# Kernel tuning notes

Measured on AMD Instinct MI355X. Metric: run time of the kernel, lower is better.

## Reference

```python
import jax, jax.numpy as jnp
import numpy as np

TAU = 1.5      # lif_tau
V_TH = 1.0     # spikingjelly default v_threshold
EPS = 1e-5     # BatchNorm eps
ALPHA = 4.0    # spikingjelly default sigmoid surrogate alpha

@jax.custom_vjp
def spike_fn(x):
    return (x >= 0.0).astype(x.dtype)

def _spike_fwd(x):
    return spike_fn(x), x

def _spike_bwd(x, g):
    s = jax.nn.sigmoid(ALPHA * x)
    return (g * ALPHA * s * (1.0 - s),)

spike_fn.defvjp(_spike_fwd, _spike_bwd)

def lif(x):
    # x: [T, B, C, N]; hard reset to 0, decay_input=True, detach_reset=True
    def step(v, xt):
        v = v + (xt - v) / TAU
        s = spike_fn(v - V_TH)
        sd = jax.lax.stop_gradient(s)
        v = (1.0 - sd) * v
        return v, s
    _, spikes = jax.lax.scan(step, jnp.zeros_like(x[0]), x)
    return spikes

def bn(x, gamma, beta, mean, var):
    # eval-mode BatchNorm1d over channel dim of [B, C, L]
    inv = gamma * jax.lax.rsqrt(var + EPS)
    return x * inv[None, :, None] + (beta - mean * inv)[None, :, None]

def setup_inputs() -> dict:
    key = jax.random.key(0)
    ks = jax.random.split(key, 13)
    B, C, T, N, H = 8, 256, 4, 4096, 1024
    return {
        "x": jax.random.normal(ks[0], (B, C, T, N), jnp.float32),
        "fc1_w": jax.random.normal(ks[1], (H, C), jnp.float32) * 0.05,
        "fc1_b": jax.random.normal(ks[2], (H,), jnp.float32) * 0.05,
        "fc2_w": jax.random.normal(ks[3], (C, H), jnp.float32) * 0.05,
        "fc2_b": jax.random.normal(ks[4], (C,), jnp.float32) * 0.05,
        "bn1_gamma": jax.random.uniform(ks[5], (H,), jnp.float32, 0.5, 1.5),
        "bn1_beta": jax.random.normal(ks[6], (H,), jnp.float32) * 0.1,
        "bn1_mean": jax.random.normal(ks[7], (H,), jnp.float32) * 0.1,
        "bn1_var": jax.random.uniform(ks[8], (H,), jnp.float32, 0.5, 1.5),
        "bn2_gamma": jax.random.uniform(ks[9], (C,), jnp.float32, 0.5, 1.5),
        "bn2_beta": jax.random.normal(ks[10], (C,), jnp.float32) * 0.1,
        "bn2_mean": jax.random.normal(ks[11], (C,), jnp.float32) * 0.1,
        "bn2_var": jax.random.uniform(ks[12], (C,), jnp.float32, 0.5, 1.5),
    }

def reference(x, fc1_w, fc1_b, fc2_w, fc2_b,
              bn1_gamma, bn1_beta, bn1_mean, bn1_var,
              bn2_gamma, bn2_beta, bn2_mean, bn2_var):
    B, C, T, N = x.shape
    H = fc1_w.shape[0]
    # fc2_bn on raw input, then LIF over T
    h = bn(x.reshape(B, C, T * N), bn2_gamma, bn2_beta, bn2_mean, bn2_var)
    h = h.reshape(B, C, T, N).transpose(2, 0, 1, 3)          # [T,B,C,N]
    h = lif(h).transpose(1, 2, 0, 3).reshape(B, C, T * N)    # [B,C,TN]
    # fc1: 1x1 conv == GEMM over channels
    h = jnp.einsum('hc,bcl->bhl', fc1_w, h) + fc1_b[None, :, None]
    h = bn(h, bn1_gamma, bn1_beta, bn1_mean, bn1_var)
    h = h.reshape(B, H, T, N).transpose(2, 0, 1, 3)          # [T,B,H,N]
    h = lif(h).transpose(1, 2, 0, 3).reshape(B, H, T * N)    # [B,H,TN]
    # fc2
    h = jnp.einsum('ch,bhl->bcl', fc2_w, h) + fc2_b[None, :, None]
    return h.reshape(B, C, T, N)
```

## Files before the change

kernel.cpp:

```cpp
#include <hip/hip_runtime.h>

#define BB 8
#define CC 256
#define TT 4
#define NNv 4096
#define HH 1024
#define LLv (TT*NNv)

typedef short bf16x8 __attribute__((ext_vector_type(8)));
typedef float f32x4 __attribute__((ext_vector_type(4)));

static __device__ __forceinline__ float bfbits2f(unsigned short h) {
    return __uint_as_float(((unsigned int)h) << 16);
}
static __device__ __forceinline__ unsigned short f2bf(float f) {
    unsigned int u = __float_as_uint(f);
    return (unsigned short)((u + 0x7FFFu + ((u >> 16) & 1u)) >> 16);
}
static __device__ __forceinline__ int permpos(int j) { return (j >> 1) + ((j & 1) << 2); }

static __device__ __forceinline__ uint4 spikes8_to_bf16(unsigned long long d) {
    unsigned int lo = (unsigned int)d, hi = (unsigned int)(d >> 32);
    uint4 o;
    o.x = (lo & 0x10001u) * 0x3F80u;
    o.y = (hi & 0x10001u) * 0x3F80u;
    o.z = ((lo >> 8) & 0x10001u) * 0x3F80u;
    o.w = ((hi >> 8) & 0x10001u) * 0x3F80u;
    return o;
}

__global__ __launch_bounds__(256) void k_prep1(const float* __restrict__ w,
                                               unsigned short* __restrict__ wf)
{
    int i = blockIdx.x * 256 + threadIdx.x;
    int h = i >> 8, c = i & 255;
    int ht = h >> 6, hr = h & 63, g = hr >> 4, ln = hr & 15;
    int ko = c >> 6, cr = c & 63, kb = cr >> 5, q = (cr >> 3) & 3, j = c & 7;
    size_t base = (((((size_t)ht * 4 + ko) * 2 + kb) * 4 + g) * 64 + q * 16 + ln) * 8 + permpos(j);
    const size_t WS = 262144;
    float x = w[i];
    unsigned short hi = f2bf(x); float r  = __fsub_rn(x, bfbits2f(hi));
    unsigned short md = f2bf(r); float r2 = __fsub_rn(r, bfbits2f(md));
    unsigned short lo = f2bf(r2);
    wf[base] = hi; wf[WS + base] = md; wf[2 * WS + base] = lo;
}

__global__ __launch_bounds__(256) void k_prep2(const float* __restrict__ w,
                                               unsigned short* __restrict__ wf)
{
    int i = blockIdx.x * 256 + threadIdx.x;
    int c = i >> 10, h = i & 1023;
    int ct = c >> 6, cr = c & 63, g = cr >> 4, ln = cr & 15;
    int ko = h >> 7, hr = h & 127, kb = hr >> 5, q = (hr >> 3) & 3, j = h & 7;
    size_t base = (((((size_t)ct * 8 + ko) * 4 + kb) * 4 + g) * 64 + q * 16 + ln) * 8 + permpos(j);
    const size_t WS = 262144;
    float x = w[i];
    unsigned short hi = f2bf(x); float r = __fsub_rn(x, bfbits2f(hi));
    unsigned short lo = f2bf(r);
    wf[base] = hi; wf[WS + base] = lo;
}

__global__ __launch_bounds__(256) void k_bn2_lif_t(
    const float* __restrict__ x,
    const float* __restrict__ g, const float* __restrict__ be,
    const float* __restrict__ mu, const float* __restrict__ va,
    unsigned char* __restrict__ s1T, int b0)
{
    __shared__ unsigned char ts[TT][64][80];
    int tx = threadIdx.x;
    int n0 = blockIdx.x * 64;
    int c0 = blockIdx.y * 64;
    int bl = blockIdx.z;
    int b  = b0 + bl;
    int cl = tx >> 2, np = tx & 3;
    int c = c0 + cl;
    float rsq = __fdiv_rn(1.0f, __fsqrt_rn(__fadd_rn(va[c], 1e-5f)));
    float inv = __fmul_rn(g[c], rsq);
    float add = __fsub_rn(be[c], __fmul_rn(mu[c], inv));
    size_t xb = ((size_t)(b * CC + c) * TT) * NNv + n0 + np * 16;
    float v[16];
    #pragma unroll
    for (int i = 0; i < 16; i++) v[i] = 0.0f;
    #pragma unroll
    for (int t = 0; t < TT; t++) {
        float4 p[4];
        #pragma unroll
        for (int k = 0; k < 4; k++) p[k] = *(const float4*)(x + xb + (size_t)t * NNv + 4 * k);
        const float* xp = (const float*)p;
        unsigned int ob[4] = {0, 0, 0, 0};
        #pragma unroll
        for (int i = 0; i < 16; i++) {
            float y = __fadd_rn(__fmul_rn(xp[i], inv), add);
            float vv = __fadd_rn(v[i], __fdiv_rn(__fsub_rn(y, v[i]), 1.5f));
            bool sp = vv >= 1.0f;
            v[i] = sp ? 0.0f : vv;
            if (sp) ob[i >> 2] |= 1u << (8 * (i & 3));
        }
        uint4 pk; pk.x = ob[0]; pk.y = ob[1]; pk.z = ob[2]; pk.w = ob[3];
        *(uint4*)&ts[t][cl][np * 16] = pk;
    }
    __syncthreads();
    int nl = tx >> 2, cp = tx & 3;
    #pragma unroll
    for (int t = 0; t < TT; t++) {
        unsigned int u[4];
        #pragma unroll
        for (int kk = 0; kk < 4; kk++) {
            u[kk] = (unsigned int)ts[t][cp * 16 + kk * 4 + 0][nl]
                  | ((unsigned int)ts[t][cp * 16 + kk * 4 + 1][nl] << 8)
                  | ((unsigned int)ts[t][cp * 16 + kk * 4 + 2][nl] << 16)
                  | ((unsigned int)ts[t][cp * 16 + kk * 4 + 3][nl] << 24);
        }
        uint4 pk; pk.x = u[0]; pk.y = u[1]; pk.z = u[2]; pk.w = u[3];
        *(uint4*)(s1T + ((size_t)(bl * TT + t) * NNv + n0 + nl) * CC + c0 + cp * 16) = pk;
    }
}

__global__ __launch_bounds__(256) void k_gemm1_lif(
    const unsigned short* __restrict__ w1f,
    const float* __restrict__ b1,
    const float* __restrict__ g1, const float* __restrict__ be1,
    const float* __restrict__ mu1, const float* __restrict__ va1,
    const unsigned char* __restrict__ s1T, unsigned char* __restrict__ s2T)
{
    __shared__ unsigned short Ss[TT][64][72];
    const int tx = threadIdx.x;
    const int n0 = blockIdx.x * 64;
    const int ht = blockIdx.y;
    const int bl = blockIdx.z;
    const int lane = tx & 63, w = tx >> 6;
    const int q = lane >> 4, ln = lane & 15;
    const int mh = (w & 1) * 32, wn = (w >> 1) * 32;
    const int h0 = ht * 64;
    const size_t WS = 262144;

    f32x4 acc[TT][2][2];
    #pragma unroll
    for (int t = 0; t < TT; t++)
    #pragma unroll
    for (int mi = 0; mi < 2; mi++)
    #pragma unroll
    for (int ni = 0; ni < 2; ni++)
        acc[t][mi][ni] = (f32x4){0.f, 0.f, 0.f, 0.f};

    for (int ko = 0; ko < 4; ko++) {
        __syncthreads();
        #pragma unroll
        for (int i = 0; i < 8; i++) {
            int task = i * 256 + tx;
            int cb = task & 7, nr = (task >> 3) & 63, t = task >> 9;
            unsigned long long d = *(const unsigned long long*)(
                s1T + ((size_t)(bl * TT + t) * NNv + n0 + nr) * CC + ko * 64 + cb * 8);
            *(uint4*)&Ss[t][nr][cb * 8] = spikes8_to_bf16(d);
        }
        __syncthreads();
        #pragma unroll
        for (int kb = 0; kb < 2; kb++) {
            bf16x8 wf[2][3];
            #pragma unroll
            for (int mi = 0; mi < 2; mi++) {
                int gg = (mh >> 4) + mi;
                size_t fbase = (((((size_t)ht * 4 + ko) * 2 + kb) * 4 + gg) * 64 + lane) * 8;
                #pragma unroll
                for (int s = 0; s < 3; s++)
                    wf[mi][s] = *(const bf16x8*)(w1f + s * WS + fbase);
            }
            #pragma unroll
            for (int t = 0; t < TT; t++) {
                bf16x8 sf0 = *(const bf16x8*)&Ss[t][wn + ln][kb * 32 + q * 8];
                bf16x8 sf1 = *(const bf16x8*)&Ss[t][wn + 16 + ln][kb * 32 + q * 8];
                #pragma unroll
                for (int s = 0; s < 3; s++) {
                    acc[t][0][0] = __builtin_amdgcn_mfma_f32_16x16x32_bf16(wf[0][s], sf0, acc[t][0][0], 0, 0, 0);
                    acc[t][0][1] = __builtin_amdgcn_mfma_f32_16x16x32_bf16(wf[0][s], sf1, acc[t][0][1], 0, 0, 0);
                    acc[t][1][0] = __builtin_amdgcn_mfma_f32_16x16x32_bf16(wf[1][s], sf0, acc[t][1][0], 0, 0, 0);
                    acc[t][1][1] = __builtin_amdgcn_mfma_f32_16x16x32_bf16(wf[1][s], sf1, acc[t][1][1], 0, 0, 0);
                }
            }
        }
    }

    #pragma unroll
    for (int mi = 0; mi < 2; mi++) {
        float invr[4], addr_[4], biasr[4];
        #pragma unroll
        for (int r = 0; r < 4; r++) {
            int h = h0 + mh + mi * 16 + q * 4 + r;
            float rsq = __fdiv_rn(1.0f, __fsqrt_rn(__fadd_rn(va1[h], 1e-5f)));
            invr[r] = __fmul_rn(g1[h], rsq);
            addr_[r] = __fsub_rn(be1[h], __fmul_rn(mu1[h], invr[r]));
            biasr[r] = b1[h];
        }
        #pragma unroll
        for (int ni = 0; ni < 2; ni++) {
            int l_n = n0 + wn + ni * 16 + ln;
            float v4[4] = {0.f, 0.f, 0.f, 0.f};
            #pragma unroll
            for (int t = 0; t < TT; t++) {
                unsigned int pk = 0;
                #pragma unroll
                for (int r = 0; r < 4; r++) {
                    float h1 = __fadd_rn(acc[t][mi][ni][r], biasr[r]);
                    float y  = __fadd_rn(__fmul_rn(h1, invr[r]), addr_[r]);
                    float vv = __fadd_rn(v4[r], __fdiv_rn(__fsub_rn(y, v4[r]), 1.5f));
                    bool sp = vv >= 1.0f;
                    v4[r] = sp ? 0.0f : vv;
                    if (sp) pk |= (1u << (8 * r));
                }
                *(unsigned int*)(s2T + ((size_t)bl * LLv + t * NNv + l_n) * HH
                                 + h0 + mh + mi * 16 + q * 4) = pk;
            }
        }
    }
}

__global__ __launch_bounds__(256) void k_gemm2(
    const unsigned short* __restrict__ w2f,
    const float* __restrict__ b2c,
    const unsigned char* __restrict__ s2T, float* __restrict__ outp, int b0)
{
    __shared__ unsigned short Ss[128][136];
    const int tx = threadIdx.x;
    const int l0 = blockIdx.x * 128;
    const int ct = blockIdx.y;
    const int bl = blockIdx.z;
    const int b  = b0 + bl;
    const int lane = tx & 63, w = tx >> 6;
    const int q = lane >> 4, ln = lane & 15;
    const int mc = (w & 1) * 32, wl = (w >> 1) * 64;
    const size_t WS = 262144;

    f32x4 acc[2][4];
    #pragma unroll
    for (int mi = 0; mi < 2; mi++)
    #pragma unroll
    for (int ni = 0; ni < 4; ni++)
        acc[mi][ni] = (f32x4){0.f, 0.f, 0.f, 0.f};

    for (int ko = 0; ko < 8; ko++) {
        __syncthreads();
        #pragma unroll
        for (int i = 0; i < 8; i++) {
            int task = i * 256 + tx;
            int hb = task & 15, lr = task >> 4;
            unsigned long long d = *(const unsigned long long*)(
                s2T + ((size_t)bl * LLv + l0 + lr) * HH + ko * 128 + hb * 8);
            *(uint4*)&Ss[lr][hb * 8] = spikes8_to_bf16(d);
        }
        __syncthreads();
        #pragma unroll
        for (int kb = 0; kb < 4; kb++) {
            bf16x8 wf[2][2];
            #pragma unroll
            for (int mi = 0; mi < 2; mi++) {
                int gg = (mc >> 4) + mi;
                size_t fbase = (((((size_t)ct * 8 + ko) * 4 + kb) * 4 + gg) * 64 + lane) * 8;
                #pragma unroll
                for (int s = 0; s < 2; s++)
                    wf[mi][s] = *(const bf16x8*)(w2f + s * WS + fbase);
            }
            bf16x8 sf[4];
            #pragma unroll
            for (int ni = 0; ni < 4; ni++)
                sf[ni] = *(const bf16x8*)&Ss[wl + ni * 16 + ln][kb * 32 + q * 8];
            #pragma unroll
            for (int s = 0; s < 2; s++)
            #pragma unroll
            for (int mi = 0; mi < 2; mi++)
            #pragma unroll
            for (int ni = 0; ni < 4; ni++)
                acc[mi][ni] = __builtin_amdgcn_mfma_f32_16x16x32_bf16(wf[mi][s], sf[ni], acc[mi][ni], 0, 0, 0);
        }
    }
    #pragma unroll
    for (int mi = 0; mi < 2; mi++)
    #pragma unroll
    for (int r = 0; r < 4; r++) {
        int c = ct * 64 + mc + mi * 16 + q * 4 + r;
        float bias = b2c[c];
        #pragma unroll
        for (int ni = 0; ni < 4; ni++) {
            int l = l0 + wl + ni * 16 + ln;
            outp[((size_t)b * CC + c) * LLv + l] = __fadd_rn(acc[mi][ni][r], bias);
        }
    }
}

extern "C" void kernel_launch(void* const* d_in, const int* in_sizes, int n_in,
                              void* d_out, int out_size, void* d_ws, size_t ws_size,
                              hipStream_t stream) {
    const float* x    = (const float*)d_in[0];
    const float* fc1w = (const float*)d_in[1];
    const float* fc1b = (const float*)d_in[2];
    const float* fc2w = (const float*)d_in[3];
    const float* fc2b = (const float*)d_in[4];
    const float* g1   = (const float*)d_in[5];
    const float* be1  = (const float*)d_in[6];
    const float* mu1  = (const float*)d_in[7];
    const float* va1  = (const float*)d_in[8];
    const float* g2   = (const float*)d_in[9];
    const float* be2  = (const float*)d_in[10];
    const float* mu2  = (const float*)d_in[11];
    const float* va2  = (const float*)d_in[12];

    const size_t WB  = (size_t)(3 + 2) * 262144 * sizeof(unsigned short);
    const size_t S1B = (size_t)TT * NNv * CC;
    const size_t S2B = (size_t)LLv * HH;

    int nbc;
    bool full_s1;
    if      (ws_size >= WB + 8 * S1B + 8 * S2B) { nbc = 8; full_s1 = true;  }
    else if (ws_size >= WB + 8 * S1B + 4 * S2B) { nbc = 4; full_s1 = true;  }
    else if (ws_size >= WB + 8 * S1B + 2 * S2B) { nbc = 2; full_s1 = true;  }
    else if (ws_size >= WB + 8 * S1B + 1 * S2B) { nbc = 1; full_s1 = true;  }
    else                                        { nbc = 1; full_s1 = false; }

    unsigned short* w1f = (unsigned short*)d_ws;
    unsigned short* w2f = w1f + (size_t)3 * 262144;
    unsigned char*  s1T = (unsigned char*)(w2f + (size_t)2 * 262144);
    unsigned char*  s2T = s1T + (full_s1 ? (size_t)8 * S1B : S1B);
    float* outp = (float*)d_out;

    hipLaunchKernelGGL(k_prep1, dim3(1024), dim3(256), 0, stream, fc1w, w1f);
    hipLaunchKernelGGL(k_prep2, dim3(1024), dim3(256), 0, stream, fc2w, w2f);

    if (full_s1) {
        hipLaunchKernelGGL(k_bn2_lif_t, dim3(NNv / 64, CC / 64, BB), dim3(256), 0, stream,
                           x, g2, be2, mu2, va2, s1T, 0);
        for (int b0 = 0; b0 < BB; b0 += nbc) {
            hipLaunchKernelGGL(k_gemm1_lif, dim3(NNv / 64, HH / 64, nbc), dim3(256), 0, stream,
                               w1f, fc1b, g1, be1, mu1, va1, s1T + (size_t)b0 * S1B, s2T);
            hipLaunchKernelGGL(k_gemm2, dim3(LLv / 128, CC / 64, nbc), dim3(256), 0, stream,
                               w2f, fc2b, s2T, outp, b0);
        }
    } else {
        for (int b0 = 0; b0 < BB; ++b0) {
            hipLaunchKernelGGL(k_bn2_lif_t, dim3(NNv / 64, CC / 64, 1), dim3(256), 0, stream,
                               x, g2, be2, mu2, va2, s1T, b0);
            hipLaunchKernelGGL(k_gemm1_lif, dim3(NNv / 64, HH / 64, 1), dim3(256), 0, stream,
                               w1f, fc1b, g1, be1, mu1, va1, s1T, s2T);
            hipLaunchKernelGGL(k_gemm2, dim3(LLv / 128, CC / 64, 1), dim3(256), 0, stream,
                               w2f, fc2b, s2T, outp, b0);
        }
    }
}
```

Measured before the change: 623.7 us.

## Double-buffer spike tiles and prefetch next K slice in both GEMMs

Both GEMM kernels now keep two LDS buffers for the spike tile and load the next K-slice from global memory into registers while the current slice is computed. Each iteration has one barrier instead of two. A custom barrier waits only on LDS counters, so the outstanding global loads stay in flight across it. The cost is doubled LDS use (lower occupancy for the gemm2 tile of about 68KB) and extra registers for the prefetched data.

```diff
diff --git a/kernel.cpp b/kernel.cpp
--- a/kernel.cpp
+++ b/kernel.cpp
@@ -27,6 +27,12 @@
     o.z = ((lo >> 8) & 0x10001u) * 0x3F80u;
     o.w = ((hi >> 8) & 0x10001u) * 0x3F80u;
     return o;
+}
+
+static __device__ __forceinline__ void barrier_keep_vmem() {
+    asm volatile("s_waitcnt lgkmcnt(0)" ::: "memory");
+    __builtin_amdgcn_s_barrier();
+    __builtin_amdgcn_sched_barrier(0);
 }
 
 __global__ __launch_bounds__(256) void k_prep1(const float* __restrict__ w,
@@ -123,7 +129,7 @@
     const float* __restrict__ mu1, const float* __restrict__ va1,
     const unsigned char* __restrict__ s1T, unsigned char* __restrict__ s2T)
 {
-    __shared__ unsigned short Ss[TT][64][72];
+    __shared__ unsigned short Ss[2][TT][64][72];
     const int tx = threadIdx.x;
     const int n0 = blockIdx.x * 64;
     const int ht = blockIdx.y;
@@ -143,17 +149,34 @@
     for (int ni = 0; ni < 2; ni++)
         acc[t][mi][ni] = (f32x4){0.f, 0.f, 0.f, 0.f};
 
+    unsigned long long d[8];
+    #pragma unroll
+    for (int i = 0; i < 8; i++) {
+        int task = i * 256 + tx;
+        int cb = task & 7, nr = (task >> 3) & 63, t = task >> 9;
+        d[i] = *(const unsigned long long*)(
+            s1T + ((size_t)(bl * TT + t) * NNv + n0 + nr) * CC + 0 * 64 + cb * 8);
+    }
+
     for (int ko = 0; ko < 4; ko++) {
-        __syncthreads();
+        const int cur = ko & 1;
         #pragma unroll
         for (int i = 0; i < 8; i++) {
             int task = i * 256 + tx;
             int cb = task & 7, nr = (task >> 3) & 63, t = task >> 9;
-            unsigned long long d = *(const unsigned long long*)(
-                s1T + ((size_t)(bl * TT + t) * NNv + n0 + nr) * CC + ko * 64 + cb * 8);
-            *(uint4*)&Ss[t][nr][cb * 8] = spikes8_to_bf16(d);
-        }
-        __syncthreads();
+            *(uint4*)&Ss[cur][t][nr][cb * 8] = spikes8_to_bf16(d[i]);
+        }
+        if (ko < 3) {
+            #pragma unroll
+            for (int i = 0; i < 8; i++) {
+                int task = i * 256 + tx;
+                int cb = task & 7, nr = (task >> 3) & 63, t = task >> 9;
+                d[i] = *(const unsigned long long*)(
+                    s1T + ((size_t)(bl * TT + t) * NNv + n0 + nr) * CC + (ko + 1) * 64 + cb * 8);
+            }
+        }
+        barrier_keep_vmem();
+
         #pragma unroll
         for (int kb = 0; kb < 2; kb++) {
             bf16x8 wf[2][3];
@@ -167,8 +190,8 @@
             }
             #pragma unroll
             for (int t = 0; t < TT; t++) {
-                bf16x8 sf0 = *(const bf16x8*)&Ss[t][wn + ln][kb * 32 + q * 8];
-                bf16x8 sf1 = *(const bf16x8*)&Ss[t][wn + 16 + ln][kb * 32 + q * 8];
+                bf16x8 sf0 = *(const bf16x8*)&Ss[cur][t][wn + ln][kb * 32 + q * 8];
+                bf16x8 sf1 = *(const bf16x8*)&Ss[cur][t][wn + 16 + ln][kb * 32 + q * 8];
                 #pragma unroll
                 for (int s = 0; s < 3; s++) {
                     acc[t][0][0] = __builtin_amdgcn_mfma_f32_16x16x32_bf16(wf[0][s], sf0, acc[t][0][0], 0, 0, 0);
@@ -219,7 +242,7 @@
     const float* __restrict__ b2c,
     const unsigned char* __restrict__ s2T, float* __restrict__ outp, int b0)
 {
-    __shared__ unsigned short Ss[128][136];
+    __shared__ unsigned short Ss[2][128][136];
     const int tx = threadIdx.x;
     const int l0 = blockIdx.x * 128;
     const int ct = blockIdx.y;
@@ -237,17 +260,34 @@
     for (int ni = 0; ni < 4; ni++)
         acc[mi][ni] = (f32x4){0.f, 0.f, 0.f, 0.f};
 
+    unsigned long long d[8];
+    #pragma unroll
+    for (int i = 0; i < 8; i++) {
+        int task = i * 256 + tx;
+        int hb = task & 15, lr = task >> 4;
+        d[i] = *(const unsigned long long*)(
+            s2T + ((size_t)bl * LLv + l0 + lr) * HH + 0 * 128 + hb * 8);
+    }
+
     for (int ko = 0; ko < 8; ko++) {
-        __syncthreads();
+        const int cur = ko & 1;
         #pragma unroll
         for (int i = 0; i < 8; i++) {
             int task = i * 256 + tx;
             int hb = task & 15, lr = task >> 4;
-            unsigned long long d = *(const unsigned long long*)(
-                s2T + ((size_t)bl * LLv + l0 + lr) * HH + ko * 128 + hb * 8);
-            *(uint4*)&Ss[lr][hb * 8] = spikes8_to_bf16(d);
-        }
-        __syncthreads();
+            *(uint4*)&Ss[cur][lr][hb * 8] = spikes8_to_bf16(d[i]);
+        }
+        if (ko < 7) {
+            #pragma unroll
+            for (int i = 0; i < 8; i++) {
+                int task = i * 256 + tx;
+                int hb = task & 15, lr = task >> 4;
+                d[i] = *(const unsigned long long*)(
+                    s2T + ((size_t)bl * LLv + l0 + lr) * HH + (ko + 1) * 128 + hb * 8);
+            }
+        }
+        barrier_keep_vmem();
+
         #pragma unroll
         for (int kb = 0; kb < 4; kb++) {
             bf16x8 wf[2][2];
@@ -262,7 +302,7 @@
             bf16x8 sf[4];
             #pragma unroll
             for (int ni = 0; ni < 4; ni++)
-                sf[ni] = *(const bf16x8*)&Ss[wl + ni * 16 + ln][kb * 32 + q * 8];
+                sf[ni] = *(const bf16x8*)&Ss[cur][wl + ni * 16 + ln][kb * 32 + q * 8];
             #pragma unroll
             for (int s = 0; s < 2; s++)
             #pragma unroll
```

New measurement: 658.5 us. +5.6%, slower.

## Replace split-bf16 MFMA GEMMs with fixed-point int8 digit-split MFMA

Applied to the files above, without the earlier changes.

The weights are quantized to fixed point (24-bit for fc1, 16-bit for fc2) and split into signed int8 digits. Both GEMMs then run on i32 16x16x64 int8 MFMA with raw 0/1 spike bytes, so spikes no longer need converting to bf16. The fc1 kernel now stages the whole spike tile once in swizzled LDS, and the fc2 kernel double-buffers its LDS with register prefetch behind a custom barrier. This doubles K per MFMA and halves LDS bytes. The cost is fixed-point quantization error in the weights, which could flip spikes near the threshold.

```diff
diff --git a/kernel.cpp b/kernel.cpp
--- a/kernel.cpp
+++ b/kernel.cpp
@@ -7,57 +7,44 @@
 #define HH 1024
 #define LLv (TT*NNv)
 
-typedef short bf16x8 __attribute__((ext_vector_type(8)));
+typedef int   int4v __attribute__((ext_vector_type(4)));
 typedef float f32x4 __attribute__((ext_vector_type(4)));
 
-static __device__ __forceinline__ float bfbits2f(unsigned short h) {
-    return __uint_as_float(((unsigned int)h) << 16);
-}
-static __device__ __forceinline__ unsigned short f2bf(float f) {
-    unsigned int u = __float_as_uint(f);
-    return (unsigned short)((u + 0x7FFFu + ((u >> 16) & 1u)) >> 16);
-}
-static __device__ __forceinline__ int permpos(int j) { return (j >> 1) + ((j & 1) << 2); }
-
-static __device__ __forceinline__ uint4 spikes8_to_bf16(unsigned long long d) {
-    unsigned int lo = (unsigned int)d, hi = (unsigned int)(d >> 32);
-    uint4 o;
-    o.x = (lo & 0x10001u) * 0x3F80u;
-    o.y = (hi & 0x10001u) * 0x3F80u;
-    o.z = ((lo >> 8) & 0x10001u) * 0x3F80u;
-    o.w = ((hi >> 8) & 0x10001u) * 0x3F80u;
-    return o;
+static __device__ __forceinline__ void barrier_keep_vmem() {
+    asm volatile("s_waitcnt lgkmcnt(0)" ::: "memory");
+    __builtin_amdgcn_s_barrier();
+    __builtin_amdgcn_sched_barrier(0);
 }
 
 __global__ __launch_bounds__(256) void k_prep1(const float* __restrict__ w,
-                                               unsigned short* __restrict__ wf)
+                                               unsigned char* __restrict__ wd)
 {
     int i = blockIdx.x * 256 + threadIdx.x;
     int h = i >> 8, c = i & 255;
-    int ht = h >> 6, hr = h & 63, g = hr >> 4, ln = hr & 15;
-    int ko = c >> 6, cr = c & 63, kb = cr >> 5, q = (cr >> 3) & 3, j = c & 7;
-    size_t base = (((((size_t)ht * 4 + ko) * 2 + kb) * 4 + g) * 64 + q * 16 + ln) * 8 + permpos(j);
-    const size_t WS = 262144;
-    float x = w[i];
-    unsigned short hi = f2bf(x); float r  = __fsub_rn(x, bfbits2f(hi));
-    unsigned short md = f2bf(r); float r2 = __fsub_rn(r, bfbits2f(md));
-    unsigned short lo = f2bf(r2);
-    wf[base] = hi; wf[WS + base] = md; wf[2 * WS + base] = lo;
+    int w24 = __float2int_rn(w[i] * 16777216.0f);
+    int d2 = ((w24 + 128) & 255) - 128;  w24 = (w24 - d2) >> 8;
+    int d1 = ((w24 + 128) & 255) - 128;  w24 = (w24 - d1) >> 8;
+    int d0 = w24;
+    size_t off = ((((size_t)(h >> 6) * 4 + (c >> 6)) * 4 + ((h >> 4) & 3)) << 10)
+               + ((c >> 4) & 3) * 256 + (h & 15) * 16 + (c & 15);
+    wd[off] = (unsigned char)d0;
+    wd[262144 + off] = (unsigned char)d1;
+    wd[2 * 262144 + off] = (unsigned char)d2;
 }
 
 __global__ __launch_bounds__(256) void k_prep2(const float* __restrict__ w,
-                                               unsigned short* __restrict__ wf)
+                                               unsigned char* __restrict__ wd)
 {
     int i = blockIdx.x * 256 + threadIdx.x;
     int c = i >> 10, h = i & 1023;
-    int ct = c >> 6, cr = c & 63, g = cr >> 4, ln = cr & 15;
-    int ko = h >> 7, hr = h & 127, kb = hr >> 5, q = (hr >> 3) & 3, j = h & 7;
-    size_t base = (((((size_t)ct * 8 + ko) * 4 + kb) * 4 + g) * 64 + q * 16 + ln) * 8 + permpos(j);
-    const size_t WS = 262144;
-    float x = w[i];
-    unsigned short hi = f2bf(x); float r = __fsub_rn(x, bfbits2f(hi));
-    unsigned short lo = f2bf(r);
-    wf[base] = hi; wf[WS + base] = lo;
+    int w16 = __float2int_rn(w[i] * 65536.0f);
+    int d1 = ((w16 + 128) & 255) - 128;  w16 = (w16 - d1) >> 8;
+    int d0 = w16;
+    size_t off = ((((((size_t)(c >> 6) * 8 + (h >> 7)) * 2 + ((h >> 6) & 1)) * 4
+                    + ((c >> 4) & 3)) << 10)
+                 + ((h >> 4) & 3) * 256 + (c & 15) * 16 + (h & 15));
+    wd[off] = (unsigned char)d0;
+    wd[262144 + off] = (unsigned char)d1;
 }
 
 __global__ __launch_bounds__(256) void k_bn2_lif_t(
@@ -117,13 +104,13 @@
 }
 
 __global__ __launch_bounds__(256) void k_gemm1_lif(
-    const unsigned short* __restrict__ w1f,
+    const unsigned char* __restrict__ w1d,
     const float* __restrict__ b1,
     const float* __restrict__ g1, const float* __restrict__ be1,
     const float* __restrict__ mu1, const float* __restrict__ va1,
     const unsigned char* __restrict__ s1T, unsigned char* __restrict__ s2T)
 {
-    __shared__ unsigned short Ss[TT][64][72];
+    __shared__ unsigned char Ls[TT * 64 * 256];
     const int tx = threadIdx.x;
     const int n0 = blockIdx.x * 64;
     const int ht = blockIdx.y;
@@ -132,53 +119,107 @@
     const int q = lane >> 4, ln = lane & 15;
     const int mh = (w & 1) * 32, wn = (w >> 1) * 32;
     const int h0 = ht * 64;
-    const size_t WS = 262144;
-
-    f32x4 acc[TT][2][2];
+
+    const int csw = ((tx & 15) ^ (tx >> 4)) << 4;
+    #pragma unroll
+    for (int half = 0; half < 2; half++) {
+        uint4 st[8];
+        #pragma unroll
+        for (int k = 0; k < 8; k++) {
+            int i = half * 8 + k;
+            int t = i >> 2, nn = (i & 3) * 16 + (tx >> 4);
+            st[k] = *(const uint4*)(s1T + ((size_t)(bl * TT + t) * NNv + n0 + nn) * CC + csw);
+        }
+        #pragma unroll
+        for (int k = 0; k < 8; k++) {
+            int i = half * 8 + k;
+            *(uint4*)&Ls[i * 4096 + tx * 16] = st[k];
+        }
+    }
+    __syncthreads();
+
+    int4v a0[TT][2][2], a1[TT][2][2];
     #pragma unroll
     for (int t = 0; t < TT; t++)
     #pragma unroll
     for (int mi = 0; mi < 2; mi++)
     #pragma unroll
+    for (int ni = 0; ni < 2; ni++) { a0[t][mi][ni] = (int4v){0,0,0,0}; a1[t][mi][ni] = (int4v){0,0,0,0}; }
+
+    #pragma unroll
+    for (int ko = 0; ko < 4; ko++) {
+        int4v sf[TT][2];
+        #pragma unroll
+        for (int t = 0; t < TT; t++)
+        #pragma unroll
+        for (int ni = 0; ni < 2; ni++)
+            sf[t][ni] = *(const int4v*)&Ls[(t * 64 + wn + ni * 16 + ln) * 256 + (((ko * 4 + q) ^ ln) << 4)];
+        int4v w0[2], w1[2];
+        #pragma unroll
+        for (int mi = 0; mi < 2; mi++) {
+            size_t fb = ((((size_t)ht * 4 + ko) * 4 + (mh >> 4) + mi) << 10) + lane * 16;
+            w0[mi] = *(const int4v*)(w1d + fb);
+            w1[mi] = *(const int4v*)(w1d + 262144 + fb);
+        }
+        #pragma unroll
+        for (int t = 0; t < TT; t++)
+        #pragma unroll
+        for (int mi = 0; mi < 2; mi++)
+        #pragma unroll
+        for (int ni = 0; ni < 2; ni++) {
+            a0[t][mi][ni] = __builtin_amdgcn_mfma_i32_16x16x64_i8(w0[mi], sf[t][ni], a0[t][mi][ni], 0, 0, 0);
+            a1[t][mi][ni] = __builtin_amdgcn_mfma_i32_16x16x64_i8(w1[mi], sf[t][ni], a1[t][mi][ni], 0, 0, 0);
+        }
+    }
+
+    f32x4 facc[TT][2][2];
+    #pragma unroll
+    for (int t = 0; t < TT; t++)
+    #pragma unroll
+    for (int mi = 0; mi < 2; mi++)
+    #pragma unroll
     for (int ni = 0; ni < 2; ni++)
-        acc[t][mi][ni] = (f32x4){0.f, 0.f, 0.f, 0.f};
-
+        facc[t][mi][ni] = __builtin_convertvector((a0[t][mi][ni] << 8) + a1[t][mi][ni], f32x4)
+                          * 1.52587890625e-05f;
+
+    int4v a2[TT][2][2];
+    #pragma unroll
+    for (int t = 0; t < TT; t++)
+    #pragma unroll
+    for (int mi = 0; mi < 2; mi++)
+    #pragma unroll
+    for (int ni = 0; ni < 2; ni++) a2[t][mi][ni] = (int4v){0,0,0,0};
+
+    #pragma unroll
     for (int ko = 0; ko < 4; ko++) {
-        __syncthreads();
-        #pragma unroll
-        for (int i = 0; i < 8; i++) {
-            int task = i * 256 + tx;
-            int cb = task & 7, nr = (task >> 3) & 63, t = task >> 9;
-            unsigned long long d = *(const unsigned long long*)(
-                s1T + ((size_t)(bl * TT + t) * NNv + n0 + nr) * CC + ko * 64 + cb * 8);
-            *(uint4*)&Ss[t][nr][cb * 8] = spikes8_to_bf16(d);
-        }
-        __syncthreads();
-        #pragma unroll
-        for (int kb = 0; kb < 2; kb++) {
-            bf16x8 wf[2][3];
-            #pragma unroll
-            for (int mi = 0; mi < 2; mi++) {
-                int gg = (mh >> 4) + mi;
-                size_t fbase = (((((size_t)ht * 4 + ko) * 2 + kb) * 4 + gg) * 64 + lane) * 8;
-                #pragma unroll
-                for (int s = 0; s < 3; s++)
-                    wf[mi][s] = *(const bf16x8*)(w1f + s * WS + fbase);
-            }
-            #pragma unroll
-            for (int t = 0; t < TT; t++) {
-                bf16x8 sf0 = *(const bf16x8*)&Ss[t][wn + ln][kb * 32 + q * 8];
-                bf16x8 sf1 = *(const bf16x8*)&Ss[t][wn + 16 + ln][kb * 32 + q * 8];
-                #pragma unroll
-                for (int s = 0; s < 3; s++) {
-                    acc[t][0][0] = __builtin_amdgcn_mfma_f32_16x16x32_bf16(wf[0][s], sf0, acc[t][0][0], 0, 0, 0);
-                    acc[t][0][1] = __builtin_amdgcn_mfma_f32_16x16x32_bf16(wf[0][s], sf1, acc[t][0][1], 0, 0, 0);
-                    acc[t][1][0] = __builtin_amdgcn_mfma_f32_16x16x32_bf16(wf[1][s], sf0, acc[t][1][0], 0, 0, 0);
-                    acc[t][1][1] = __builtin_amdgcn_mfma_f32_16x16x32_bf16(wf[1][s], sf1, acc[t][1][1], 0, 0, 0);
-                }
-            }
-        }
-    }
+        int4v sf[TT][2];
+        #pragma unroll
+        for (int t = 0; t < TT; t++)
+        #pragma unroll
+        for (int ni = 0; ni < 2; ni++)
+            sf[t][ni] = *(const int4v*)&Ls[(t * 64 + wn + ni * 16 + ln) * 256 + (((ko * 4 + q) ^ ln) << 4)];
+        int4v w2[2];
+        #pragma unroll
+        for (int mi = 0; mi < 2; mi++) {
+            size_t fb = ((((size_t)ht * 4 + ko) * 4 + (mh >> 4) + mi) << 10) + lane * 16;
+            w2[mi] = *(const int4v*)(w1d + 2 * 262144 + fb);
+        }
+        #pragma unroll
+        for (int t = 0; t < TT; t++)
+        #pragma unroll
+        for (int mi = 0; mi < 2; mi++)
+        #pragma unroll
+        for (int ni = 0; ni < 2; ni++)
+            a2[t][mi][ni] = __builtin_amdgcn_mfma_i32_16x16x64_i8(w2[mi], sf[t][ni], a2[t][mi][ni], 0, 0, 0);
+    }
+    #pragma unroll
+    for (int t = 0; t < TT; t++)
+    #pragma unroll
+    for (int mi = 0; mi < 2; mi++)
+    #pragma unroll
+    for (int ni = 0; ni < 2; ni++)
+        facc[t][mi][ni] = facc[t][mi][ni]
+            + __builtin_convertvector(a2[t][mi][ni], f32x4) * 5.9604644775390625e-08f;
 
     #pragma unroll
     for (int mi = 0; mi < 2; mi++) {
@@ -200,7 +241,7 @@
                 unsigned int pk = 0;
                 #pragma unroll
                 for (int r = 0; r < 4; r++) {
-                    float h1 = __fadd_rn(acc[t][mi][ni][r], biasr[r]);
+                    float h1 = __fadd_rn(facc[t][mi][ni][r], biasr[r]);
                     float y  = __fadd_rn(__fmul_rn(h1, invr[r]), addr_[r]);
                     float vv = __fadd_rn(v4[r], __fdiv_rn(__fsub_rn(y, v4[r]), 1.5f));
                     bool sp = vv >= 1.0f;
@@ -215,11 +256,11 @@
 }
 
 __global__ __launch_bounds__(256) void k_gemm2(
-    const unsigned short* __restrict__ w2f,
+    const unsigned char* __restrict__ w2d,
     const float* __restrict__ b2c,
     const unsigned char* __restrict__ s2T, float* __restrict__ outp, int b0)
 {
-    __shared__ unsigned short Ss[128][136];
+    __shared__ unsigned char Ls[2 * 128 * 128];
     const int tx = threadIdx.x;
     const int l0 = blockIdx.x * 128;
     const int ct = blockIdx.y;
@@ -228,60 +269,69 @@
     const int lane = tx & 63, w = tx >> 6;
     const int q = lane >> 4, ln = lane & 15;
     const int mc = (w & 1) * 32, wl = (w >> 1) * 64;
-    const size_t WS = 262144;
-
-    f32x4 acc[2][4];
-    #pragma unroll
-    for (int mi = 0; mi < 2; mi++)
-    #pragma unroll
-    for (int ni = 0; ni < 4; ni++)
-        acc[mi][ni] = (f32x4){0.f, 0.f, 0.f, 0.f};
+
+    int4v acc[2][2][4];
+    #pragma unroll
+    for (int d = 0; d < 2; d++)
+    #pragma unroll
+    for (int mi = 0; mi < 2; mi++)
+    #pragma unroll
+    for (int ni = 0; ni < 4; ni++) acc[d][mi][ni] = (int4v){0,0,0,0};
+
+    const int hsw = ((tx & 7) ^ ((tx >> 3) & 7)) << 4;
+    uint4 sg[4];
+    #pragma unroll
+    for (int i = 0; i < 4; i++)
+        sg[i] = *(const uint4*)(s2T + ((size_t)bl * LLv + l0 + i * 32 + (tx >> 3)) * HH + hsw);
 
     for (int ko = 0; ko < 8; ko++) {
-        __syncthreads();
-        #pragma unroll
-        for (int i = 0; i < 8; i++) {
-            int task = i * 256 + tx;
-            int hb = task & 15, lr = task >> 4;
-            unsigned long long d = *(const unsigned long long*)(
-                s2T + ((size_t)bl * LLv + l0 + lr) * HH + ko * 128 + hb * 8);
-            *(uint4*)&Ss[lr][hb * 8] = spikes8_to_bf16(d);
-        }
-        __syncthreads();
-        #pragma unroll
-        for (int kb = 0; kb < 4; kb++) {
-            bf16x8 wf[2][2];
+        const int cur = ko & 1;
+        #pragma unroll
+        for (int i = 0; i < 4; i++)
+            *(uint4*)&Ls[cur * 16384 + i * 4096 + tx * 16] = sg[i];
+        if (ko < 7) {
+            #pragma unroll
+            for (int i = 0; i < 4; i++)
+                sg[i] = *(const uint4*)(s2T + ((size_t)bl * LLv + l0 + i * 32 + (tx >> 3)) * HH
+                                        + (ko + 1) * 128 + hsw);
+        }
+        barrier_keep_vmem();
+
+        #pragma unroll
+        for (int kb = 0; kb < 2; kb++) {
+            int4v wf[2][2];
+            #pragma unroll
+            for (int d = 0; d < 2; d++)
             #pragma unroll
             for (int mi = 0; mi < 2; mi++) {
-                int gg = (mc >> 4) + mi;
-                size_t fbase = (((((size_t)ct * 8 + ko) * 4 + kb) * 4 + gg) * 64 + lane) * 8;
-                #pragma unroll
-                for (int s = 0; s < 2; s++)
-                    wf[mi][s] = *(const bf16x8*)(w2f + s * WS + fbase);
+                size_t fb = ((((((size_t)ct * 8 + ko) * 2 + kb) * 4 + (mc >> 4) + mi)) << 10) + lane * 16;
+                wf[d][mi] = *(const int4v*)(w2d + (size_t)d * 262144 + fb);
             }
-            bf16x8 sf[4];
+            int4v sf[4];
             #pragma unroll
             for (int ni = 0; ni < 4; ni++)
-                sf[ni] = *(const bf16x8*)&Ss[wl + ni * 16 + ln][kb * 32 + q * 8];
-            #pragma unroll
-            for (int s = 0; s < 2; s++)
+                sf[ni] = *(const int4v*)&Ls[cur * 16384 + (wl + ni * 16 + ln) * 128
+                                            + (((kb * 4 + q) ^ (ln & 7)) << 4)];
+            #pragma unroll
+            for (int d = 0; d < 2; d++)
             #pragma unroll
             for (int mi = 0; mi < 2; mi++)
             #pragma unroll
             for (int ni = 0; ni < 4; ni++)
-                acc[mi][ni] = __builtin_amdgcn_mfma_f32_16x16x32_bf16(wf[mi][s], sf[ni], acc[mi][ni], 0, 0, 0);
-        }
-    }
-    #pragma unroll
-    for (int mi = 0; mi < 2; mi++)
-    #pragma unroll
-    for (int r = 0; r < 4; r++) {
-        int c = ct * 64 + mc + mi * 16 + q * 4 + r;
-        float bias = b2c[c];
-        #pragma unroll
-        for (int ni = 0; ni < 4; ni++) {
+                acc[d][mi][ni] = __builtin_amdgcn_mfma_i32_16x16x64_i8(wf[d][mi], sf[ni], acc[d][mi][ni], 0, 0, 0);
+        }
+    }
+    #pragma unroll
+    for (int mi = 0; mi < 2; mi++)
+    #pragma unroll
+    for (int ni = 0; ni < 4; ni++) {
+        int4v tv = (acc[0][mi][ni] << 8) + acc[1][mi][ni];
+        #pragma unroll
+        for (int r = 0; r < 4; r++) {
+            int c = ct * 64 + mc + mi * 16 + q * 4 + r;
             int l = l0 + wl + ni * 16 + ln;
-            outp[((size_t)b * CC + c) * LLv + l] = __fadd_rn(acc[mi][ni][r], bias);
+            outp[((size_t)b * CC + c) * LLv + l] =
+                __fadd_rn(__fmul_rn((float)tv[r], 1.52587890625e-05f), b2c[c]);
         }
     }
 }
@@ -303,7 +353,7 @@
     const float* mu2  = (const float*)d_in[11];
     const float* va2  = (const float*)d_in[12];
 
-    const size_t WB  = (size_t)(3 + 2) * 262144 * sizeof(unsigned short);
+    const size_t WB  = (size_t)3 * 262144 + (size_t)2 * 262144;
     const size_t S1B = (size_t)TT * NNv * CC;
     const size_t S2B = (size_t)LLv * HH;
 
@@ -315,32 +365,32 @@
     else if (ws_size >= WB + 8 * S1B + 1 * S2B) { nbc = 1; full_s1 = true;  }
     else                                        { nbc = 1; full_s1 = false; }
 
-    unsigned short* w1f = (unsigned short*)d_ws;
-    unsigned short* w2f = w1f + (size_t)3 * 262144;
-    unsigned char*  s1T = (unsigned char*)(w2f + (size_t)2 * 262144);
-    unsigned char*  s2T = s1T + (full_s1 ? (size_t)8 * S1B : S1B);
+    unsigned char* w1d = (unsigned char*)d_ws;
+    unsigned char* w2d = w1d + (size_t)3 * 262144;
+    unsigned char* s1T = w2d + (size_t)2 * 262144;
+    unsigned char* s2T = s1T + (full_s1 ? (size_t)8 * S1B : S1B);
     float* outp = (float*)d_out;
 
-    hipLaunchKernelGGL(k_prep1, dim3(1024), dim3(256), 0, stream, fc1w, w1f);
-    hipLaunchKernelGGL(k_prep2, dim3(1024), dim3(256), 0, stream, fc2w, w2f);
+    hipLaunchKernelGGL(k_prep1, dim3(1024), dim3(256), 0, stream, fc1w, w1d);
+    hipLaunchKernelGGL(k_prep2, dim3(1024), dim3(256), 0, stream, fc2w, w2d);
 
     if (full_s1) {
         hipLaunchKernelGGL(k_bn2_lif_t, dim3(NNv / 64, CC / 64, BB), dim3(256), 0, stream,
                            x, g2, be2, mu2, va2, s1T, 0);
         for (int b0 = 0; b0 < BB; b0 += nbc) {
             hipLaunchKernelGGL(k_gemm1_lif, dim3(NNv / 64, HH / 64, nbc), dim3(256), 0, stream,
-                               w1f, fc1b, g1, be1, mu1, va1, s1T + (size_t)b0 * S1B, s2T);
+                               w1d, fc1b, g1, be1, mu1, va1, s1T + (size_t)b0 * S1B, s2T);
             hipLaunchKernelGGL(k_gemm2, dim3(LLv / 128, CC / 64, nbc), dim3(256), 0, stream,
-                               w2f, fc2b, s2T, outp, b0);
+                               w2d, fc2b, s2T, outp, b0);
         }
     } else {
         for (int b0 = 0; b0 < BB; ++b0) {
             hipLaunchKernelGGL(k_bn2_lif_t, dim3(NNv / 64, CC / 64, 1), dim3(256), 0, stream,
                                x, g2, be2, mu2, va2, s1T, b0);
             hipLaunchKernelGGL(k_gemm1_lif, dim3(NNv / 64, HH / 64, 1), dim3(256), 0, stream,
-                               w1f, fc1b, g1, be1, mu1, va1, s1T, s2T);
+                               w1d, fc1b, g1, be1, mu1, va1, s1T, s2T);
             hipLaunchKernelGGL(k_gemm2, dim3(LLv / 128, CC / 64, 1), dim3(256), 0, stream,
-                               w2f, fc2b, s2T, outp, b0);
-        }
-    }
-}
+                               w2d, fc2b, s2T, outp, b0);
+        }
+    }
+}
```

Result: slower. 690.0 us (+10.6%).

## Load spike operands directly into MFMA registers, dropping LDS staging and barriers

Applied to the files above, without the earlier changes.

Both GEMM kernels stop staging spike tiles through shared memory. Each lane now loads its own 8-byte spike fragment from global memory, expands it to bf16 in registers, and prefetches the next k-step's fragment one phase ahead (register double buffering). The intent is to remove LDS traffic and __syncthreads barriers and to raise occupancy, with launch_bounds asking for 3 blocks per CU. In exchange, global loads become narrow and strided with no reuse across warps: each spike row is fetched by multiple warps and relies on L1/L2 for reuse, and register pressure rises.

```diff
diff --git a/kernel.cpp b/kernel.cpp
--- a/kernel.cpp
+++ b/kernel.cpp
@@ -116,14 +116,13 @@
     }
 }
 
-__global__ __launch_bounds__(256) void k_gemm1_lif(
+__global__ __launch_bounds__(256, 3) void k_gemm1_lif(
     const unsigned short* __restrict__ w1f,
     const float* __restrict__ b1,
     const float* __restrict__ g1, const float* __restrict__ be1,
     const float* __restrict__ mu1, const float* __restrict__ va1,
     const unsigned char* __restrict__ s1T, unsigned char* __restrict__ s2T)
 {
-    __shared__ unsigned short Ss[TT][64][72];
     const int tx = threadIdx.x;
     const int n0 = blockIdx.x * 64;
     const int ht = blockIdx.y;
@@ -143,42 +142,59 @@
     for (int ni = 0; ni < 2; ni++)
         acc[t][mi][ni] = (f32x4){0.f, 0.f, 0.f, 0.f};
 
-    for (int ko = 0; ko < 4; ko++) {
-        __syncthreads();
-        #pragma unroll
-        for (int i = 0; i < 8; i++) {
-            int task = i * 256 + tx;
-            int cb = task & 7, nr = (task >> 3) & 63, t = task >> 9;
-            unsigned long long d = *(const unsigned long long*)(
-                s1T + ((size_t)(bl * TT + t) * NNv + n0 + nr) * CC + ko * 64 + cb * 8);
-            *(uint4*)&Ss[t][nr][cb * 8] = spikes8_to_bf16(d);
-        }
-        __syncthreads();
-        #pragma unroll
-        for (int kb = 0; kb < 2; kb++) {
-            bf16x8 wf[2][3];
-            #pragma unroll
-            for (int mi = 0; mi < 2; mi++) {
-                int gg = (mh >> 4) + mi;
-                size_t fbase = (((((size_t)ht * 4 + ko) * 2 + kb) * 4 + gg) * 64 + lane) * 8;
-                #pragma unroll
-                for (int s = 0; s < 3; s++)
-                    wf[mi][s] = *(const bf16x8*)(w1f + s * WS + fbase);
+    const unsigned char* sb = s1T + ((size_t)(bl * TT) * NNv + (n0 + wn + ln)) * CC + q * 8;
+#define SOFF1(t, ni, ko, kb) ((size_t)(t) * NNv * CC + (size_t)(ni) * 16 * CC + (ko) * 64 + (kb) * 32)
+
+    unsigned long long dc[TT][2], dn[TT][2];
+    #pragma unroll
+    for (int t = 0; t < TT; t++)
+    #pragma unroll
+    for (int ni = 0; ni < 2; ni++)
+        dc[t][ni] = *(const unsigned long long*)(sb + SOFF1(t, ni, 0, 0));
+
+    #pragma unroll
+    for (int ph = 0; ph < 8; ph++) {
+        const int ko = ph >> 1, kb = ph & 1;
+        if (ph < 7) {
+            const int ko2 = (ph + 1) >> 1, kb2 = (ph + 1) & 1;
+            #pragma unroll
+            for (int t = 0; t < TT; t++)
+            #pragma unroll
+            for (int ni = 0; ni < 2; ni++)
+                dn[t][ni] = *(const unsigned long long*)(sb + SOFF1(t, ni, ko2, kb2));
+        }
+        bf16x8 wf[2][3];
+        #pragma unroll
+        for (int mi = 0; mi < 2; mi++) {
+            int gg = (mh >> 4) + mi;
+            size_t fbase = (((((size_t)ht * 4 + ko) * 2 + kb) * 4 + gg) * 64 + lane) * 8;
+            #pragma unroll
+            for (int s = 0; s < 3; s++)
+                wf[mi][s] = *(const bf16x8*)(w1f + s * WS + fbase);
+        }
+        #pragma unroll
+        for (int t = 0; t < TT; t++) {
+            uint4 e0 = spikes8_to_bf16(dc[t][0]);
+            uint4 e1 = spikes8_to_bf16(dc[t][1]);
+            bf16x8 sf0 = *(bf16x8*)&e0;
+            bf16x8 sf1 = *(bf16x8*)&e1;
+            #pragma unroll
+            for (int s = 0; s < 3; s++) {
+                acc[t][0][0] = __builtin_amdgcn_mfma_f32_16x16x32_bf16(wf[0][s], sf0, acc[t][0][0], 0, 0, 0);
+                acc[t][0][1] = __builtin_amdgcn_mfma_f32_16x16x32_bf16(wf[0][s], sf1, acc[t][0][1], 0, 0, 0);
+                acc[t][1][0] = __builtin_amdgcn_mfma_f32_16x16x32_bf16(wf[1][s], sf0, acc[t][1][0], 0, 0, 0);
+                acc[t][1][1] = __builtin_amdgcn_mfma_f32_16x16x32_bf16(wf[1][s], sf1, acc[t][1][1], 0, 0, 0);
             }
-            #pragma unroll
-            for (int t = 0; t < TT; t++) {
-                bf16x8 sf0 = *(const bf16x8*)&Ss[t][wn + ln][kb * 32 + q * 8];
-                bf16x8 sf1 = *(const bf16x8*)&Ss[t][wn + 16 + ln][kb * 32 + q * 8];
-                #pragma unroll
-                for (int s = 0; s < 3; s++) {
-                    acc[t][0][0] = __builtin_amdgcn_mfma_f32_16x16x32_bf16(wf[0][s], sf0, acc[t][0][0], 0, 0, 0);
-                    acc[t][0][1] = __builtin_amdgcn_mfma_f32_16x16x32_bf16(wf[0][s], sf1, acc[t][0][1], 0, 0, 0);
-                    acc[t][1][0] = __builtin_amdgcn_mfma_f32_16x16x32_bf16(wf[1][s], sf0, acc[t][1][0], 0, 0, 0);
-                    acc[t][1][1] = __builtin_amdgcn_mfma_f32_16x16x32_bf16(wf[1][s], sf1, acc[t][1][1], 0, 0, 0);
-                }
-            }
-        }
-    }
+        }
+        if (ph < 7) {
+            #pragma unroll
+            for (int t = 0; t < TT; t++)
+            #pragma unroll
+            for (int ni = 0; ni < 2; ni++)
+                dc[t][ni] = dn[t][ni];
+        }
+    }
+#undef SOFF1
 
     #pragma unroll
     for (int mi = 0; mi < 2; mi++) {
@@ -214,12 +230,11 @@
     }
 }
 
-__global__ __launch_bounds__(256) void k_gemm2(
+__global__ __launch_bounds__(256, 3) void k_gemm2(
     const unsigned short* __restrict__ w2f,
     const float* __restrict__ b2c,
     const unsigned char* __restrict__ s2T, float* __restrict__ outp, int b0)
 {
-    __shared__ unsigned short Ss[128][136];
     const int tx = threadIdx.x;
     const int l0 = blockIdx.x * 128;
     const int ct = blockIdx.y;
@@ -237,41 +252,53 @@
     for (int ni = 0; ni < 4; ni++)
         acc[mi][ni] = (f32x4){0.f, 0.f, 0.f, 0.f};
 
-    for (int ko = 0; ko < 8; ko++) {
-        __syncthreads();
-        #pragma unroll
-        for (int i = 0; i < 8; i++) {
-            int task = i * 256 + tx;
-            int hb = task & 15, lr = task >> 4;
-            unsigned long long d = *(const unsigned long long*)(
-                s2T + ((size_t)bl * LLv + l0 + lr) * HH + ko * 128 + hb * 8);
-            *(uint4*)&Ss[lr][hb * 8] = spikes8_to_bf16(d);
-        }
-        __syncthreads();
-        #pragma unroll
-        for (int kb = 0; kb < 4; kb++) {
-            bf16x8 wf[2][2];
-            #pragma unroll
-            for (int mi = 0; mi < 2; mi++) {
-                int gg = (mc >> 4) + mi;
-                size_t fbase = (((((size_t)ct * 8 + ko) * 4 + kb) * 4 + gg) * 64 + lane) * 8;
-                #pragma unroll
-                for (int s = 0; s < 2; s++)
-                    wf[mi][s] = *(const bf16x8*)(w2f + s * WS + fbase);
-            }
-            bf16x8 sf[4];
+    const unsigned char* sb = s2T + ((size_t)bl * LLv + l0 + wl + ln) * HH + q * 8;
+#define SOFF2(ni, ko, kb) ((size_t)(ni) * 16 * HH + (ko) * 128 + (kb) * 32)
+
+    unsigned long long dc[4], dn[4];
+    #pragma unroll
+    for (int ni = 0; ni < 4; ni++)
+        dc[ni] = *(const unsigned long long*)(sb + SOFF2(ni, 0, 0));
+
+    #pragma unroll
+    for (int ph = 0; ph < 32; ph++) {
+        const int ko = ph >> 2, kb = ph & 3;
+        if (ph < 31) {
+            const int ko2 = (ph + 1) >> 2, kb2 = (ph + 1) & 3;
             #pragma unroll
             for (int ni = 0; ni < 4; ni++)
-                sf[ni] = *(const bf16x8*)&Ss[wl + ni * 16 + ln][kb * 32 + q * 8];
+                dn[ni] = *(const unsigned long long*)(sb + SOFF2(ni, ko2, kb2));
+        }
+        bf16x8 wf[2][2];
+        #pragma unroll
+        for (int mi = 0; mi < 2; mi++) {
+            int gg = (mc >> 4) + mi;
+            size_t fbase = (((((size_t)ct * 8 + ko) * 4 + kb) * 4 + gg) * 64 + lane) * 8;
             #pragma unroll
             for (int s = 0; s < 2; s++)
-            #pragma unroll
-            for (int mi = 0; mi < 2; mi++)
+                wf[mi][s] = *(const bf16x8*)(w2f + s * WS + fbase);
+        }
+        bf16x8 sf[4];
+        #pragma unroll
+        for (int ni = 0; ni < 4; ni++) {
+            uint4 e = spikes8_to_bf16(dc[ni]);
+            sf[ni] = *(bf16x8*)&e;
+        }
+        #pragma unroll
+        for (int s = 0; s < 2; s++)
+        #pragma unroll
+        for (int mi = 0; mi < 2; mi++)
+        #pragma unroll
+        for (int ni = 0; ni < 4; ni++)
+            acc[mi][ni] = __builtin_amdgcn_mfma_f32_16x16x32_bf16(wf[mi][s], sf[ni], acc[mi][ni], 0, 0, 0);
+        if (ph < 31) {
             #pragma unroll
             for (int ni = 0; ni < 4; ni++)
-                acc[mi][ni] = __builtin_amdgcn_mfma_f32_16x16x32_bf16(wf[mi][s], sf[ni], acc[mi][ni], 0, 0, 0);
-        }
-    }
+                dc[ni] = dn[ni];
+        }
+    }
+#undef SOFF2
+
     #pragma unroll
     for (int mi = 0; mi < 2; mi++)
     #pragma unroll
```

Result: slower. 892.0 us (+43.0%).
